# Kernel optimization log

Measured on AMD Instinct MI355X. Metric: run time of the kernel, lower is better.

The kernel has to match this reference:

```python
import jax, jax.numpy as jnp
import numpy as np

B, V, H = 128, 50257, 2048   # batch, vocab, history length
NEG_INF = jnp.float32(-jnp.inf)
TEMP_MIN = 1e-5


def setup_inputs() -> dict:
    key = jax.random.key(0)
    k1, k2, k3 = jax.random.split(key, 3)
    logits = jax.random.normal(k1, (B, V), jnp.float32) * 4.0
    previous_tokens = jax.random.randint(k2, (B, H), 0, V)
    # uniform noise for the exponential-race (Gumbel-max) draw; strictly positive
    u = jax.random.uniform(k3, (B, V), jnp.float32, minval=1e-10, maxval=1.0)
    return {
        "logits": logits,
        "previous_tokens": previous_tokens,
        "u": u,
        "top_p": jnp.full((1,), 0.9, jnp.float32),
        "repetition_penalty": jnp.full((1,), 1.35, jnp.float32),
        "temperature": jnp.full((1,), 0.7, jnp.float32),
        "top_k": 50,
    }


def _logits_to_probs(logits, previous_tokens, temperature, top_k, top_p, repetition_penalty):
    b = jnp.arange(logits.shape[0])[:, None]  # [B,1] row index for scatters
    # repetition penalty: gather history scores, shrink, scatter back
    score = jnp.take_along_axis(logits, previous_tokens, axis=1)          # [B,H]
    score = jnp.where(score < 0, score * repetition_penalty, score / repetition_penalty)
    logits = logits.at[b, previous_tokens].set(score)                     # [B,V]
    # nucleus (top-p) filtering via descending sort + cumulative softmax
    order = jnp.argsort(-logits, axis=-1)                                 # [B,V]
    sorted_logits = jnp.take_along_axis(logits, order, axis=1)
    cum_probs = jnp.cumsum(jax.nn.softmax(sorted_logits, axis=-1), axis=-1)
    remove_sorted = cum_probs > top_p
    remove_sorted = remove_sorted.at[:, 0].set(False)                     # keep best token
    # scatter removal mask back to vocab order (order is a permutation)
    remove = jnp.zeros_like(remove_sorted).at[b, order].set(remove_sorted)
    logits = jnp.where(remove, NEG_INF, logits)
    # temperature + top-k pivot filter
    logits = logits / jnp.maximum(temperature, TEMP_MIN)
    v = jax.lax.top_k(logits, top_k)[0]                                   # [B,top_k]
    pivot = v[:, -1:]
    logits = jnp.where(logits < pivot, NEG_INF, logits)
    return jax.nn.softmax(logits, axis=-1)


def reference(logits, previous_tokens, u, top_p, repetition_penalty, temperature, top_k):
    previous_tokens = previous_tokens.astype(jnp.int32)
    probs = _logits_to_probs(logits, previous_tokens, temperature, top_k, top_p,
                             repetition_penalty)
    # multinomial_sample_one_no_sync: exponential race argmax(probs / Exp(1))
    q = -jnp.log(u)
    idx_next = jnp.argmax(probs / q, axis=-1, keepdims=True).astype(jnp.int32)
    return idx_next, probs
```

## Files before the change

### kernel.cpp

```cpp
#include <hip/hip_runtime.h>
#include <cfloat>
#include <cmath>
#include <cstdint>

#define VV 50257
#define SPLITS 8
#define CHUNKA 6284
#define BMW ((CHUNKA + 31) / 32)
#define CAPC 1024
#define K1T 256
#define NWAVE (K1T / 64)
#define K2T 512
#define CEXP 28.0f

__device__ __forceinline__ unsigned fmono(float f) {
    unsigned b = __float_as_uint(f);
    return b ^ (((int)b < 0) ? 0xFFFFFFFFu : 0x80000000u);
}
__device__ __forceinline__ float unmono(unsigned m) {
    unsigned b = (m & 0x80000000u) ? (m ^ 0x80000000u) : ~m;
    return __uint_as_float(b);
}
__device__ __forceinline__ uint64_t mkkey(unsigned mono, int idx) {
    return ((uint64_t)mono << 32) | (unsigned)(~idx);
}

__device__ __forceinline__ void proc_el(
    float x, int gi, bool pen, float rp, float inv_rp, float& s,
    uint64_t& k0, uint64_t& k1, uint64_t& k2, uint64_t& k3)
{
    if (pen) x = (x < 0.f) ? x * rp : x * inv_rp;
    s += __expf(x - CEXP);
    uint64_t a = mkkey(fmono(x), gi);
    if (a > k3) {
        uint64_t n0 = (k0 > a) ? k0 : a;
        uint64_t m0 = (k0 > a) ? a : k0;
        uint64_t n1 = (k1 > m0) ? k1 : m0;
        uint64_t m1 = (k1 > m0) ? m0 : k1;
        uint64_t n2 = (k2 > m1) ? k2 : m1;
        uint64_t m2 = (k2 > m1) ? m1 : k2;
        k0 = n0; k1 = n1; k2 = n2; k3 = m2;
    }
}

__global__ __launch_bounds__(K1T) void pp_k1(
    const float* __restrict__ logits, const int* __restrict__ prev,
    const float* __restrict__ rpp,
    float* __restrict__ ps, uint64_t* __restrict__ gkey,
    float* __restrict__ out_probs, int Hp)
{
    const int sp = blockIdx.x, row = blockIdx.y;
    const int tid = threadIdx.x, lane = tid & 63, wid = tid >> 6;
    const int c0 = sp * CHUNKA;
    const int c1 = min(VV, c0 + CHUNKA);
    const int len = c1 - c0;
    const float rp = rpp[0], inv_rp = 1.0f / rp;

    __shared__ unsigned bm[BMW];
    __shared__ uint64_t kls[K1T];
    __shared__ uint64_t cand[CAPC];
    __shared__ uint64_t top64[64];
    __shared__ float red_s[NWAVE];
    __shared__ uint64_t sV64;
    __shared__ int sCnt, sCnt2;

    for (int i = tid; i < BMW; i += K1T) bm[i] = 0u;
    if (tid == 0) sCnt = 0;
    __syncthreads();

    const int* prow = prev + (size_t)row * Hp;
    const int h4 = Hp >> 2;
    const int4* prow4 = (const int4*)prow;
    for (int i = tid; i < h4; i += K1T) {
        int4 t4 = prow4[i];
        int t;
        t = t4.x; if (t >= c0 && t < c1) { int o = t - c0; atomicOr(&bm[o >> 5], 1u << (o & 31)); }
        t = t4.y; if (t >= c0 && t < c1) { int o = t - c0; atomicOr(&bm[o >> 5], 1u << (o & 31)); }
        t = t4.z; if (t >= c0 && t < c1) { int o = t - c0; atomicOr(&bm[o >> 5], 1u << (o & 31)); }
        t = t4.w; if (t >= c0 && t < c1) { int o = t - c0; atomicOr(&bm[o >> 5], 1u << (o & 31)); }
    }
    for (int i = 4 * h4 + tid; i < Hp; i += K1T) {
        int t = prow[i];
        if (t >= c0 && t < c1) { int o = t - c0; atomicOr(&bm[o >> 5], 1u << (o & 31)); }
    }
    __syncthreads();

    const float* lrow = logits + (size_t)row * VV;
    float* orow = out_probs + (size_t)row * VV;
    const int pad = (4 - (row & 3)) & 3;
    const int n4 = (len - pad) >> 2;
    const int tail0 = pad + 4 * n4;
    const float4* l4 = (const float4*)(lrow + c0 + pad);
    float4* o4 = (float4*)(orow + c0 + pad);
    const float4 z4 = make_float4(0.f, 0.f, 0.f, 0.f);

    auto keyAt = [&](int o) -> uint64_t {
        float x = lrow[c0 + o];
        if ((bm[o >> 5] >> (o & 31)) & 1u) x = (x < 0.f) ? x * rp : x * inv_rp;
        return mkkey(fmono(x), c0 + o);
    };

    float s = 0.0f;
    uint64_t k0 = 0ull, k1 = 0ull, k2 = 0ull, k3 = 0ull;
    for (int o = tid; o < pad; o += K1T) {
        float x = lrow[c0 + o];
        orow[c0 + o] = 0.0f;
        proc_el(x, c0 + o, (bm[o >> 5] >> (o & 31)) & 1u, rp, inv_rp, s, k0, k1, k2, k3);
    }
    #pragma unroll 4
    for (int k = tid; k < n4; k += K1T) {
        float4 v = l4[k];
        o4[k] = z4;
        const int ob = pad + 4 * k;
        proc_el(v.x, c0 + ob + 0, (bm[(ob+0) >> 5] >> ((ob+0) & 31)) & 1u, rp, inv_rp, s, k0, k1, k2, k3);
        proc_el(v.y, c0 + ob + 1, (bm[(ob+1) >> 5] >> ((ob+1) & 31)) & 1u, rp, inv_rp, s, k0, k1, k2, k3);
        proc_el(v.z, c0 + ob + 2, (bm[(ob+2) >> 5] >> ((ob+2) & 31)) & 1u, rp, inv_rp, s, k0, k1, k2, k3);
        proc_el(v.w, c0 + ob + 3, (bm[(ob+3) >> 5] >> ((ob+3) & 31)) & 1u, rp, inv_rp, s, k0, k1, k2, k3);
    }
    for (int o = tail0 + tid; o < len; o += K1T) {
        float x = lrow[c0 + o];
        orow[c0 + o] = 0.0f;
        proc_el(x, c0 + o, (bm[o >> 5] >> (o & 31)) & 1u, rp, inv_rp, s, k0, k1, k2, k3);
    }

    #pragma unroll
    for (int off = 32; off; off >>= 1) s += __shfl_down(s, off);
    if (lane == 0) red_s[wid] = s;

    {
        uint64_t v = k0;
        #pragma unroll
        for (int kk = 2; kk <= 64; kk <<= 1) {
            #pragma unroll
            for (int j = kk >> 1; j > 0; j >>= 1) {
                uint64_t o = __shfl_xor(v, j);
                bool lower = (lane & j) == 0;
                bool asc = (lane & kk) == 0;
                uint64_t mx = (v > o) ? v : o;
                uint64_t mn = (v > o) ? o : v;
                v = (lower != asc) ? mx : mn;
            }
        }
        kls[wid * 64 + (63 - lane)] = v;
    }
    __syncthreads();

    const int slot = row * SPLITS + sp;
    if (tid == 0) {
        float S = red_s[0];
        #pragma unroll
        for (int w = 1; w < NWAVE; ++w) S += red_s[w];
        ps[slot] = S;
    }

    {
        const uint64_t ki = kls[tid];
        int r = tid & 63;
        const int j = tid >> 6;
        #pragma unroll
        for (int o = 0; o < NWAVE; ++o) {
            if (o == j) continue;
            const uint64_t* ls = &kls[o * 64];
            int lo = 0, hi = 64;
            while (lo < hi) {
                int mid = (lo + hi) >> 1;
                if (ls[mid] > ki) lo = mid + 1; else hi = mid;
            }
            r += lo;
        }
        if (r == 63) sV64 = ki;
    }
    __syncthreads();
    const uint64_t th = sV64;

    if (k3 < th) {
        if (k0 >= th) { int p = atomicAdd(&sCnt, 1); if (p < CAPC) cand[p] = k0; }
        if (k1 >= th) { int p = atomicAdd(&sCnt, 1); if (p < CAPC) cand[p] = k1; }
        if (k2 >= th) { int p = atomicAdd(&sCnt, 1); if (p < CAPC) cand[p] = k2; }
    } else {
        for (int o = tid; o < pad; o += K1T) {
            uint64_t a = keyAt(o);
            if (a >= th) { int p = atomicAdd(&sCnt, 1); if (p < CAPC) cand[p] = a; }
        }
        for (int k = tid; k < n4; k += K1T) {
            const int ob = pad + 4 * k;
            #pragma unroll
            for (int jj = 0; jj < 4; ++jj) {
                uint64_t a = keyAt(ob + jj);
                if (a >= th) { int p = atomicAdd(&sCnt, 1); if (p < CAPC) cand[p] = a; }
            }
        }
        for (int o = tail0 + tid; o < len; o += K1T) {
            uint64_t a = keyAt(o);
            if (a >= th) { int p = atomicAdd(&sCnt, 1); if (p < CAPC) cand[p] = a; }
        }
    }
    __syncthreads();
    int cnt = min(sCnt, CAPC);

    if (sCnt > CAPC) {
        uint64_t loK = th, hiK = ~0ull, thF = th;
        bool ok = false;
        for (int it = 0; it < 64 && !ok; ++it) {
            uint64_t mid = loK + ((hiK - loK) >> 1);
            if (mid == loK) { thF = loK; break; }
            if (tid == 0) sCnt2 = 0;
            __syncthreads();
            int lc = 0;
            for (int o = tid; o < pad; o += K1T) lc += (int)(keyAt(o) >= mid);
            for (int k = tid; k < n4; k += K1T) {
                const int ob = pad + 4 * k;
                #pragma unroll
                for (int jj = 0; jj < 4; ++jj) lc += (int)(keyAt(ob + jj) >= mid);
            }
            for (int o = tail0 + tid; o < len; o += K1T) lc += (int)(keyAt(o) >= mid);
            #pragma unroll
            for (int off = 32; off; off >>= 1) lc += __shfl_down(lc, off);
            if (lane == 0) atomicAdd(&sCnt2, lc);
            __syncthreads();
            int c = sCnt2;
            if (c >= 64 && c <= CAPC) { thF = mid; ok = true; }
            else if (c > CAPC) loK = mid;
            else hiK = mid;
            __syncthreads();
        }
        if (tid == 0) sCnt = 0;
        __syncthreads();
        for (int o = tid; o < pad; o += K1T) {
            uint64_t a = keyAt(o);
            if (a >= thF) { int p = atomicAdd(&sCnt, 1); if (p < CAPC) cand[p] = a; }
        }
        for (int k = tid; k < n4; k += K1T) {
            const int ob = pad + 4 * k;
            #pragma unroll
            for (int jj = 0; jj < 4; ++jj) {
                uint64_t a = keyAt(ob + jj);
                if (a >= thF) { int p = atomicAdd(&sCnt, 1); if (p < CAPC) cand[p] = a; }
            }
        }
        for (int o = tail0 + tid; o < len; o += K1T) {
            uint64_t a = keyAt(o);
            if (a >= thF) { int p = atomicAdd(&sCnt, 1); if (p < CAPC) cand[p] = a; }
        }
        __syncthreads();
        cnt = min(sCnt, CAPC);
    }

    for (int t = tid; t < cnt; t += K1T) {
        const uint64_t ki = cand[t];
        int r = 0;
        int j = 0;
        for (; j + 8 <= cnt; j += 8) {
            uint64_t a0 = cand[j],   a1 = cand[j+1], a2 = cand[j+2], a3 = cand[j+3];
            uint64_t a4 = cand[j+4], a5 = cand[j+5], a6 = cand[j+6], a7 = cand[j+7];
            r += (int)(a0 > ki) + (int)(a1 > ki) + (int)(a2 > ki) + (int)(a3 > ki)
               + (int)(a4 > ki) + (int)(a5 > ki) + (int)(a6 > ki) + (int)(a7 > ki);
        }
        for (; j < cnt; ++j) r += (int)(cand[j] > ki);
        if (r < 64) top64[r] = ki;
    }
    __syncthreads();
    if (tid < 64) gkey[(size_t)slot * 64 + tid] = top64[tid];
}

__global__ __launch_bounds__(K2T) void pp_k2(
    const float* __restrict__ u, const float* __restrict__ toppp,
    const float* __restrict__ tempp, const int* __restrict__ topkp,
    const float* __restrict__ ps, const uint64_t* __restrict__ gkey,
    float* __restrict__ out_idx, float* __restrict__ out_probs)
{
    const int row = blockIdx.x, tid = threadIdx.x;
    __shared__ uint64_t ck[SPLITS * 64];
    __shared__ uint64_t tk[64];
    __shared__ float sS;

    ck[tid] = gkey[(size_t)row * (SPLITS * 64) + tid];
    if (tid == 0) {
        float S = 0.0f;
        #pragma unroll
        for (int j = 0; j < SPLITS; ++j) S += ps[row * SPLITS + j];
        sS = S;
    }
    __syncthreads();

    {
        const int j = tid >> 6;
        const uint64_t ki = ck[tid];
        int r = tid & 63;
        #pragma unroll
        for (int o = 0; o < SPLITS; ++o) {
            if (o == j) continue;
            const uint64_t* ls = &ck[o * 64];
            int lo = 0, hi = 64;
            while (lo < hi) {
                int mid = (lo + hi) >> 1;
                if (ls[mid] > ki) lo = mid + 1; else hi = mid;
            }
            r += lo;
        }
        if (r < 64) tk[r] = ki;
    }
    __syncthreads();

    if (tid < 64) {
        const int lane = tid;
        const float top_p = toppp[0];
        const float temp = tempp[0];
        int K = topkp[0]; K = min(max(K, 1), 64);
        const float Ssum = sS;
        const uint64_t k64 = tk[lane];
        const float vl = unmono((unsigned)(k64 >> 32));
        const int ci = (int)(~(unsigned)(k64 & 0xFFFFFFFFu));
        bool act = (lane < K);
        float e = act ? expf(vl - CEXP) / Ssum : 0.0f;
        float cum = e;
        #pragma unroll
        for (int off2 = 1; off2 < 64; off2 <<= 1) {
            float pv = __shfl_up(cum, off2);
            if (lane >= off2) cum += pv;
        }
        unsigned long long bal = __ballot(act && (cum <= top_p));
        int n = (int)__popcll(bal);
        if (n < 1) n = 1;
        const float v0 = __shfl(vl, 0);
        const float invT = 1.0f / fmaxf(temp, 1e-5f);
        bool keep = (lane < n);
        float w = keep ? expf((vl - v0) * invT) : 0.0f;
        float Z = w;
        #pragma unroll
        for (int off2 = 32; off2; off2 >>= 1) Z += __shfl_xor(Z, off2);
        float p = keep ? (w / Z) : 0.0f;
        if (keep) out_probs[(size_t)row * VV + ci] = p;
        float ratio = -1.0f;
        if (keep) ratio = p / (-logf(u[(size_t)row * VV + ci]));
        int bi = keep ? ci : 0x7FFFFFFF;
        #pragma unroll
        for (int off2 = 32; off2; off2 >>= 1) {
            float orat = __shfl_xor(ratio, off2);
            int oidx = __shfl_xor(bi, off2);
            if (orat > ratio || (orat == ratio && oidx < bi)) { ratio = orat; bi = oidx; }
        }
        if (lane == 0) out_idx[row] = (float)bi;
    }
}

extern "C" void kernel_launch(void* const* d_in, const int* in_sizes, int n_in,
                              void* d_out, int out_size, void* d_ws, size_t ws_size,
                              hipStream_t stream) {
    const float* logits = (const float*)d_in[0];
    const int*   prev   = (const int*)d_in[1];
    const float* u      = (const float*)d_in[2];
    const float* topp   = (const float*)d_in[3];
    const float* rp     = (const float*)d_in[4];
    const float* temp   = (const float*)d_in[5];
    const int*   topk   = (const int*)d_in[6];

    const int B  = in_sizes[0] / VV;
    const int Hp = in_sizes[1] / B;

    char* ws = (char*)d_ws;
    float* ps = (float*)ws;
    uint64_t* gkey = (uint64_t*)(ws + 16384);

    float* out = (float*)d_out;
    pp_k1<<<dim3(SPLITS, B), K1T, 0, stream>>>(
        logits, prev, rp, ps, gkey, out + B, Hp);
    pp_k2<<<B, K2T, 0, stream>>>(
        u, topp, temp, topk, ps, gkey, out, out + B);
}
```

Before: 34.98 us.

## Cache penalized logits in LDS and simplify per-thread top key tracking

Penalized logits for each chunk are staged in a shared-memory array, so the candidate collection pass and any threshold refinement read LDS instead of re-reading global memory. The per-thread top-4 insertion network is reduced to a single running max, and the candidate capacity drops from 1024 to 256. The output zeroing stores move after the main scan. In exchange, a per-thread max gives a looser threshold, so more elements pass it and the bisection fallback may run more often. The extra ~25KB of LDS may also lower occupancy.

```diff
diff --git a/kernel.cpp b/kernel.cpp
--- a/kernel.cpp
+++ b/kernel.cpp
@@ -7,7 +7,7 @@
 #define SPLITS 8
 #define CHUNKA 6284
 #define BMW ((CHUNKA + 31) / 32)
-#define CAPC 1024
+#define CAPC 256
 #define K1T 256
 #define NWAVE (K1T / 64)
 #define K2T 512
@@ -23,24 +23,6 @@
 }
 __device__ __forceinline__ uint64_t mkkey(unsigned mono, int idx) {
     return ((uint64_t)mono << 32) | (unsigned)(~idx);
-}
-
-__device__ __forceinline__ void proc_el(
-    float x, int gi, bool pen, float rp, float inv_rp, float& s,
-    uint64_t& k0, uint64_t& k1, uint64_t& k2, uint64_t& k3)
-{
-    if (pen) x = (x < 0.f) ? x * rp : x * inv_rp;
-    s += __expf(x - CEXP);
-    uint64_t a = mkkey(fmono(x), gi);
-    if (a > k3) {
-        uint64_t n0 = (k0 > a) ? k0 : a;
-        uint64_t m0 = (k0 > a) ? a : k0;
-        uint64_t n1 = (k1 > m0) ? k1 : m0;
-        uint64_t m1 = (k1 > m0) ? m0 : k1;
-        uint64_t n2 = (k2 > m1) ? k2 : m1;
-        uint64_t m2 = (k2 > m1) ? m1 : k2;
-        k0 = n0; k1 = n1; k2 = n2; k3 = m2;
-    }
 }
 
 __global__ __launch_bounds__(K1T) void pp_k1(
@@ -57,6 +39,7 @@
     const float rp = rpp[0], inv_rp = 1.0f / rp;
 
     __shared__ unsigned bm[BMW];
+    __shared__ float vals[CHUNKA];
     __shared__ uint64_t kls[K1T];
     __shared__ uint64_t cand[CAPC];
     __shared__ uint64_t top64[64];
@@ -94,33 +77,41 @@
     float4* o4 = (float4*)(orow + c0 + pad);
     const float4 z4 = make_float4(0.f, 0.f, 0.f, 0.f);
 
-    auto keyAt = [&](int o) -> uint64_t {
+    float s = 0.0f;
+    uint64_t k0 = 0ull;
+    for (int o = tid; o < pad; o += K1T) {
         float x = lrow[c0 + o];
         if ((bm[o >> 5] >> (o & 31)) & 1u) x = (x < 0.f) ? x * rp : x * inv_rp;
-        return mkkey(fmono(x), c0 + o);
-    };
-
-    float s = 0.0f;
-    uint64_t k0 = 0ull, k1 = 0ull, k2 = 0ull, k3 = 0ull;
-    for (int o = tid; o < pad; o += K1T) {
-        float x = lrow[c0 + o];
-        orow[c0 + o] = 0.0f;
-        proc_el(x, c0 + o, (bm[o >> 5] >> (o & 31)) & 1u, rp, inv_rp, s, k0, k1, k2, k3);
+        vals[o] = x;
+        s += __expf(x - CEXP);
+        uint64_t a = mkkey(fmono(x), c0 + o);
+        k0 = (a > k0) ? a : k0;
     }
     #pragma unroll 4
     for (int k = tid; k < n4; k += K1T) {
         float4 v = l4[k];
-        o4[k] = z4;
         const int ob = pad + 4 * k;
-        proc_el(v.x, c0 + ob + 0, (bm[(ob+0) >> 5] >> ((ob+0) & 31)) & 1u, rp, inv_rp, s, k0, k1, k2, k3);
-        proc_el(v.y, c0 + ob + 1, (bm[(ob+1) >> 5] >> ((ob+1) & 31)) & 1u, rp, inv_rp, s, k0, k1, k2, k3);
-        proc_el(v.z, c0 + ob + 2, (bm[(ob+2) >> 5] >> ((ob+2) & 31)) & 1u, rp, inv_rp, s, k0, k1, k2, k3);
-        proc_el(v.w, c0 + ob + 3, (bm[(ob+3) >> 5] >> ((ob+3) & 31)) & 1u, rp, inv_rp, s, k0, k1, k2, k3);
+        float x;
+        x = v.x; if ((bm[(ob+0) >> 5] >> ((ob+0) & 31)) & 1u) x = (x < 0.f) ? x * rp : x * inv_rp;
+        vals[ob + 0] = x; s += __expf(x - CEXP);
+        { uint64_t a = mkkey(fmono(x), c0 + ob + 0); k0 = (a > k0) ? a : k0; }
+        x = v.y; if ((bm[(ob+1) >> 5] >> ((ob+1) & 31)) & 1u) x = (x < 0.f) ? x * rp : x * inv_rp;
+        vals[ob + 1] = x; s += __expf(x - CEXP);
+        { uint64_t a = mkkey(fmono(x), c0 + ob + 1); k0 = (a > k0) ? a : k0; }
+        x = v.z; if ((bm[(ob+2) >> 5] >> ((ob+2) & 31)) & 1u) x = (x < 0.f) ? x * rp : x * inv_rp;
+        vals[ob + 2] = x; s += __expf(x - CEXP);
+        { uint64_t a = mkkey(fmono(x), c0 + ob + 2); k0 = (a > k0) ? a : k0; }
+        x = v.w; if ((bm[(ob+3) >> 5] >> ((ob+3) & 31)) & 1u) x = (x < 0.f) ? x * rp : x * inv_rp;
+        vals[ob + 3] = x; s += __expf(x - CEXP);
+        { uint64_t a = mkkey(fmono(x), c0 + ob + 3); k0 = (a > k0) ? a : k0; }
     }
     for (int o = tail0 + tid; o < len; o += K1T) {
         float x = lrow[c0 + o];
-        orow[c0 + o] = 0.0f;
-        proc_el(x, c0 + o, (bm[o >> 5] >> (o & 31)) & 1u, rp, inv_rp, s, k0, k1, k2, k3);
+        if ((bm[o >> 5] >> (o & 31)) & 1u) x = (x < 0.f) ? x * rp : x * inv_rp;
+        vals[o] = x;
+        s += __expf(x - CEXP);
+        uint64_t a = mkkey(fmono(x), c0 + o);
+        k0 = (a > k0) ? a : k0;
     }
 
     #pragma unroll
@@ -173,74 +164,52 @@
     __syncthreads();
     const uint64_t th = sV64;
 
-    if (k3 < th) {
-        if (k0 >= th) { int p = atomicAdd(&sCnt, 1); if (p < CAPC) cand[p] = k0; }
-        if (k1 >= th) { int p = atomicAdd(&sCnt, 1); if (p < CAPC) cand[p] = k1; }
-        if (k2 >= th) { int p = atomicAdd(&sCnt, 1); if (p < CAPC) cand[p] = k2; }
-    } else {
-        for (int o = tid; o < pad; o += K1T) {
-            uint64_t a = keyAt(o);
-            if (a >= th) { int p = atomicAdd(&sCnt, 1); if (p < CAPC) cand[p] = a; }
-        }
-        for (int k = tid; k < n4; k += K1T) {
-            const int ob = pad + 4 * k;
-            #pragma unroll
-            for (int jj = 0; jj < 4; ++jj) {
-                uint64_t a = keyAt(ob + jj);
-                if (a >= th) { int p = atomicAdd(&sCnt, 1); if (p < CAPC) cand[p] = a; }
-            }
-        }
-        for (int o = tail0 + tid; o < len; o += K1T) {
-            uint64_t a = keyAt(o);
-            if (a >= th) { int p = atomicAdd(&sCnt, 1); if (p < CAPC) cand[p] = a; }
-        }
-    }
-    __syncthreads();
-    int cnt = min(sCnt, CAPC);
-
-    if (sCnt > CAPC) {
-        uint64_t loK = th, hiK = ~0ull, thF = th;
-        bool ok = false;
-        for (int it = 0; it < 64 && !ok; ++it) {
+    for (int o = tid; o < len; o += K1T) {
+        float x = vals[o];
+        uint64_t a = mkkey(fmono(x), c0 + o);
+        if (a >= th) {
+            int p = atomicAdd(&sCnt, 1);
+            if (p < CAPC) cand[p] = a;
+        }
+    }
+    __syncthreads();
+    int cnt = sCnt;
+
+    for (int o = tid; o < pad; o += K1T) orow[c0 + o] = 0.0f;
+    for (int k = tid; k < n4; k += K1T) o4[k] = z4;
+    for (int o = tail0 + tid; o < len; o += K1T) orow[c0 + o] = 0.0f;
+
+    if (cnt > CAPC) {
+        uint64_t loK = th, hiK = ~0ull;
+        uint64_t thF = th;
+        for (int it = 0; it < 64; ++it) {
             uint64_t mid = loK + ((hiK - loK) >> 1);
-            if (mid == loK) { thF = loK; break; }
+            if (mid == loK) { thF = hiK; break; }
             if (tid == 0) sCnt2 = 0;
             __syncthreads();
             int lc = 0;
-            for (int o = tid; o < pad; o += K1T) lc += (int)(keyAt(o) >= mid);
-            for (int k = tid; k < n4; k += K1T) {
-                const int ob = pad + 4 * k;
-                #pragma unroll
-                for (int jj = 0; jj < 4; ++jj) lc += (int)(keyAt(ob + jj) >= mid);
-            }
-            for (int o = tail0 + tid; o < len; o += K1T) lc += (int)(keyAt(o) >= mid);
+            for (int o = tid; o < len; o += K1T) {
+                float x = vals[o];
+                lc += (int)(mkkey(fmono(x), c0 + o) >= mid);
+            }
             #pragma unroll
             for (int off = 32; off; off >>= 1) lc += __shfl_down(lc, off);
             if (lane == 0) atomicAdd(&sCnt2, lc);
             __syncthreads();
             int c = sCnt2;
-            if (c >= 64 && c <= CAPC) { thF = mid; ok = true; }
-            else if (c > CAPC) loK = mid;
-            else hiK = mid;
             __syncthreads();
+            if (c >= 64 && c <= CAPC) { thF = mid; break; }
+            if (c > CAPC) loK = mid; else hiK = mid;
         }
         if (tid == 0) sCnt = 0;
         __syncthreads();
-        for (int o = tid; o < pad; o += K1T) {
-            uint64_t a = keyAt(o);
-            if (a >= thF) { int p = atomicAdd(&sCnt, 1); if (p < CAPC) cand[p] = a; }
-        }
-        for (int k = tid; k < n4; k += K1T) {
-            const int ob = pad + 4 * k;
-            #pragma unroll
-            for (int jj = 0; jj < 4; ++jj) {
-                uint64_t a = keyAt(ob + jj);
-                if (a >= thF) { int p = atomicAdd(&sCnt, 1); if (p < CAPC) cand[p] = a; }
-            }
-        }
-        for (int o = tail0 + tid; o < len; o += K1T) {
-            uint64_t a = keyAt(o);
-            if (a >= thF) { int p = atomicAdd(&sCnt, 1); if (p < CAPC) cand[p] = a; }
+        for (int o = tid; o < len; o += K1T) {
+            float x = vals[o];
+            uint64_t a = mkkey(fmono(x), c0 + o);
+            if (a >= thF) {
+                int p = atomicAdd(&sCnt, 1);
+                if (p < CAPC) cand[p] = a;
+            }
         }
         __syncthreads();
         cnt = min(sCnt, CAPC);
```

New measurement: 31.89 us. 8.8% less time.
